# Kernel tuning notes

Hardware: AMD Instinct MI355X
Metric: run time of the kernel (lower is better)

The kernel has to match this reference:

```python
import jax, jax.numpy as jnp
import numpy as np

B, S, D = 1, 2048, 4096
H, KVH, HD = 32, 8, 128
ROPE_THETA = 10000.0
RMS_EPS = 1e-5


def setup_inputs() -> dict:
    key = jax.random.key(0)
    k1, k2, k3 = jax.random.split(key, 3)
    scale = 1.0 / np.sqrt(D)
    return {
        "inputs_embeds": jax.random.normal(k1, (B, S, D), dtype=jnp.float32),
        "attention_mask": jnp.ones((B, S), dtype=jnp.float32),
        "g": jnp.ones((D,), dtype=jnp.float32),
        "Wq": jax.random.normal(k2, (D, H * HD), dtype=jnp.float32) * scale,
        "Wk": jax.random.normal(k3, (D, KVH * HD), dtype=jnp.float32) * scale,
    }


def _rotate_half(x):
    return jnp.concatenate([-x[..., HD // 2:], x[..., :HD // 2]], axis=-1)


def reference(inputs_embeds, attention_mask, g, Wq, Wk):
    # RMSNorm
    var = jnp.mean(jnp.square(inputs_embeds), axis=-1, keepdims=True)
    h = inputs_embeds * jax.lax.rsqrt(var + RMS_EPS) * g

    # QK projections -> [B, heads, S, HD]
    q = (h @ Wq).reshape(B, S, H, HD).transpose(0, 2, 1, 3)
    k = (h @ Wk).reshape(B, S, KVH, HD).transpose(0, 2, 1, 3)

    # RoPE (llama-style: cos/sin of duplicated half-dim freqs)
    pos = jnp.arange(S, dtype=jnp.float32)
    inv_freq = 1.0 / (ROPE_THETA ** (jnp.arange(0, HD, 2, dtype=jnp.float32) / HD))
    freqs = pos[:, None] * inv_freq[None, :]            # [S, HD/2]
    emb = jnp.concatenate([freqs, freqs], axis=-1)       # [S, HD]
    cos = jnp.cos(emb)[None, None]                       # [1,1,S,HD]
    sin = jnp.sin(emb)[None, None]
    q = q * cos + _rotate_half(q) * sin
    k = k * cos + _rotate_half(k) * sin

    # repeat_kv: expand KV heads to H query heads (grouped-query)
    k = jnp.repeat(k, H // KVH, axis=1)                  # [B,H,S,HD]

    # raw QK^T scores (no softmax/V)
    scores = jnp.einsum('bhqd,bhkd->bhqk', q, k) / np.float32(np.sqrt(HD))

    # causal mask + 2D padding mask (all-ones here -> pure causal)
    min_f = jnp.finfo(scores.dtype).min
    i = jnp.arange(S)[:, None]
    j = jnp.arange(S)[None, :]
    causal = jnp.where(j > i, min_f, jnp.float32(0.0))   # [S,S]
    pad = (causal[None, None] == 0.0) & (attention_mask[:, None, None, :] == 0.0)
    mask = jnp.where(pad, min_f, causal[None, None])     # [B,1,S,S]
    return scores + mask
```

## Files before the change

kernel.cpp:

```cpp
#include <hip/hip_runtime.h>
#include <hip/hip_bf16.h>
#include <math.h>

#define S_LEN 2048
#define D_DIM 4096
#define NTOT 5120

typedef _Float16 f16x8 __attribute__((ext_vector_type(8)));
typedef float f32x4 __attribute__((ext_vector_type(4)));

#define MASKF (-3.3895313892515355e+38f)

#define QCH_BASE 134217728ull
#define KCH_BASE 201326592ull

__device__ __forceinline__ void async_ld16(const void* g, void* l) {
  __builtin_amdgcn_global_load_lds((const __attribute__((address_space(1))) void*)g,
                                   (__attribute__((address_space(3))) void*)l, 16, 0, 0);
}

__global__ void rope_tables(float* __restrict__ ct, float* __restrict__ st) {
  int i = blockIdx.x * 256 + threadIdx.x;
  int s = i >> 6, f = i & 63;
  float inv = (float)(1.0 / pow(10000.0, (double)(2 * f) / 128.0));
  float ang = (float)s * inv;
  ct[i] = (float)cos((double)ang);
  st[i] = (float)sin((double)ang);
}

__global__ __launch_bounds__(256) void rmsnorm_cast(const float* __restrict__ x,
                                                    const float* __restrict__ g,
                                                    _Float16* __restrict__ h) {
  int s = blockIdx.x;
  int t = threadIdx.x, w = t >> 6, l = t & 63;
  const f32x4* xr = (const f32x4*)(x + (size_t)s * D_DIM);
  const f32x4* gr = (const f32x4*)g;
  f32x4 v[4];
  float ss = 0.f;
#pragma unroll
  for (int i = 0; i < 4; ++i) {
    v[i] = xr[t + i * 256];
    ss += v[i][0] * v[i][0] + v[i][1] * v[i][1] + v[i][2] * v[i][2] + v[i][3] * v[i][3];
  }
#pragma unroll
  for (int off = 32; off; off >>= 1) ss += __shfl_down(ss, off);
  __shared__ float red[4];
  if (l == 0) red[w] = ss;
  __syncthreads();
  float tot = red[0] + red[1] + red[2] + red[3];
  float scale = rsqrtf(tot * (1.f / D_DIM) + 1e-5f);
  _Float16* hr = h + (size_t)s * D_DIM;
#pragma unroll
  for (int i = 0; i < 4; ++i) {
    f32x4 gg = gr[t + i * 256];
    _Float16 o[4];
    o[0] = (_Float16)(v[i][0] * scale * gg[0]);
    o[1] = (_Float16)(v[i][1] * scale * gg[1]);
    o[2] = (_Float16)(v[i][2] * scale * gg[2]);
    o[3] = (_Float16)(v[i][3] * scale * gg[3]);
    *(short4*)(hr + (size_t)(t + i * 256) * 4) = *(short4*)o;
  }
}

__global__ __launch_bounds__(256) void transpose_cast(const float* __restrict__ W,
                                                      _Float16* __restrict__ Wt, int N) {
  __shared__ float tile[32][33];
  int ntiles = N >> 5;
  int tn = blockIdx.x % ntiles, td = blockIdx.x / ntiles;
  int c = threadIdx.x & 31, r0 = threadIdx.x >> 5;
  int d0 = td * 32, n0 = tn * 32;
#pragma unroll
  for (int i = 0; i < 4; ++i) {
    int r = r0 + i * 8;
    tile[r][c] = W[(size_t)(d0 + r) * N + n0 + c];
  }
  __syncthreads();
#pragma unroll
  for (int i = 0; i < 4; ++i) {
    int r = r0 + i * 8;
    Wt[(size_t)(n0 + r) * D_DIM + d0 + c] = (_Float16)tile[c][r];
  }
}

__global__ __launch_bounds__(256, 2) void gemm_bt_f16(const _Float16* __restrict__ A,
                                                      const _Float16* __restrict__ Bt,
                                                      _Float16* __restrict__ C, int N, int K) {
  __shared__ _Float16 As[128 * 64];
  __shared__ _Float16 Bs[128 * 64];
  const int tid = threadIdx.x, w = tid >> 6, l = tid & 63;
  const int brow = blockIdx.y * 128, bcol = blockIdx.x * 128;
  const int wr = (w >> 1) * 64, wc = (w & 1) * 64;
  f32x4 acc[4][4] = {};

  int st_o[4], st_r[4], st_src[4];
#pragma unroll
  for (int p = 0; p < 4; ++p) {
    int ob = (p * 4 + w) * 1024;
    int o = ob + l * 16;
    int r = o >> 7;
    int slot = (o >> 4) & 7;
    st_o[p] = ob; st_r[p] = r; st_src[p] = slot ^ (r & 7);
  }

  for (int k0 = 0; k0 < K; k0 += 64) {
#pragma unroll
    for (int p = 0; p < 4; ++p) {
      async_ld16(A + (size_t)(brow + st_r[p]) * K + (k0 + st_src[p] * 8), (char*)As + st_o[p]);
      async_ld16(Bt + (size_t)(bcol + st_r[p]) * K + (k0 + st_src[p] * 8), (char*)Bs + st_o[p]);
    }
    asm volatile("s_waitcnt vmcnt(0)" ::: "memory");
    __syncthreads();
#pragma unroll
    for (int ks = 0; ks < 2; ++ks) {
      int kslot = ks * 4 + (l >> 4);
      f16x8 af[4], bf[4];
#pragma unroll
      for (int m = 0; m < 4; ++m) {
        int row = wr + m * 16 + (l & 15);
        af[m] = *(const f16x8*)((const char*)As + row * 128 + ((kslot ^ (row & 7)) << 4));
      }
#pragma unroll
      for (int n = 0; n < 4; ++n) {
        int row = wc + n * 16 + (l & 15);
        bf[n] = *(const f16x8*)((const char*)Bs + row * 128 + ((kslot ^ (row & 7)) << 4));
      }
#pragma unroll
      for (int m = 0; m < 4; ++m)
#pragma unroll
        for (int n = 0; n < 4; ++n)
          acc[m][n] = __builtin_amdgcn_mfma_f32_16x16x32_f16(af[m], bf[n], acc[m][n], 0, 0, 0);
    }
    __syncthreads();
  }
  const int colb = bcol + wc + (l & 15);
  const int rowb = brow + wr + ((l >> 4) << 2);
#pragma unroll
  for (int m = 0; m < 4; ++m)
#pragma unroll
    for (int n = 0; n < 4; ++n) {
      size_t base = (size_t)(rowb + m * 16) * N + (colb + n * 16);
#pragma unroll
      for (int j = 0; j < 4; ++j) C[base + (size_t)j * N] = (_Float16)acc[m][n][j];
    }
}

__global__ void rope_chunk(const _Float16* __restrict__ src, const float* __restrict__ ct,
                           const float* __restrict__ st, char* __restrict__ base) {
  int b = blockIdx.x;
  int s = b / 40, h = b % 40;
  int d = threadIdx.x;
  float v = (float)src[(size_t)s * NTOT + h * 128 + d];
  float p = (float)src[(size_t)s * NTOT + h * 128 + (d ^ 64)];
  float c = ct[s * 64 + (d & 63)];
  float sn = st[s * 64 + (d & 63)];
  float o = v * c + ((d < 64) ? -p : p) * sn;
  size_t byte;
  if (h < 32) {
    int cc = 2 * s + (h >> 4);
    byte = QCH_BASE + (size_t)(cc >> 10) * 16777216ull + (size_t)(cc & 1023) * 8192ull +
           4096ull + (size_t)((h & 15) * 128 + d) * 2;
  } else {
    int kv = h - 32;
    byte = KCH_BASE + (size_t)(s >> 1) * 8192ull + 4096ull + (size_t)(s & 1) * 2048ull +
           (size_t)(kv * 128 + d) * 2;
  }
  *(_Float16*)(base + byte) = (_Float16)o;
}

__device__ __forceinline__ void fill_tile_f32(float* __restrict__ outh, int qi, int kj) {
  f32x4 mv = {MASKF, MASKF, MASKF, MASKF};
  int rr = threadIdx.x >> 5, cc = threadIdx.x & 31;
#pragma unroll
  for (int i = 0; i < 16; ++i) {
    int r = qi * 128 + i * 8 + rr;
    ((f32x4*)(outh + (size_t)r * S_LEN + kj * 128))[cc] = mv;
  }
}

__global__ __launch_bounds__(256, 2) void qk_full(const char* __restrict__ base,
                                                  const float* __restrict__ am,
                                                  float* __restrict__ out) {
  __shared__ _Float16 Qs[128 * 128], Ks[128 * 128];
  const int h = blockIdx.y;
  const int qi = blockIdx.x >> 4, kj = blockIdx.x & 15;
  if (h >= 8 && h <= 12 && qi < 8 && kj >= 8) return;
  float* outh = out + (size_t)h * S_LEN * S_LEN;
  if (kj > qi) { fill_tile_f32(outh, qi, kj); return; }

  const int tid = threadIdx.x, w = tid >> 6, l = tid & 63;
  const int wr = (w >> 1) * 64, wc = (w & 1) * 64;
  const int hb = h >> 4;
  const size_t hoff = (size_t)(h & 15) * 256;
  const size_t kvoff = (size_t)(h >> 2) * 256;
#pragma unroll
  for (int p = 0; p < 8; ++p) {
    int ob = (p * 4 + w) * 1024;
    int o = ob + l * 16;
    int r = o >> 8;
    int slot = (o >> 4) & 15;
    int src = slot ^ (r & 7);
    int s = qi * 128 + r;
    int cc = 2 * s + hb;
    const char* qa = base + QCH_BASE + (size_t)(cc >> 10) * 16777216ull +
                     (size_t)(cc & 1023) * 8192ull + 4096ull + hoff + src * 16;
    int s2 = kj * 128 + r;
    const char* ka = base + KCH_BASE + (size_t)(s2 >> 1) * 8192ull + 4096ull +
                     (size_t)(s2 & 1) * 2048ull + kvoff + src * 16;
    async_ld16(qa, (char*)Qs + ob);
    async_ld16(ka, (char*)Ks + ob);
  }
  asm volatile("s_waitcnt vmcnt(0)" ::: "memory");
  __syncthreads();

  f32x4 acc[4][4] = {};
#pragma unroll
  for (int ks = 0; ks < 4; ++ks) {
    int kslot = ks * 4 + (l >> 4);
    f16x8 af[4], bf[4];
#pragma unroll
    for (int m = 0; m < 4; ++m) {
      int row = wr + m * 16 + (l & 15);
      af[m] = *(const f16x8*)((const char*)Qs + row * 256 + ((kslot ^ (row & 7)) << 4));
    }
#pragma unroll
    for (int n = 0; n < 4; ++n) {
      int row = wc + n * 16 + (l & 15);
      bf[n] = *(const f16x8*)((const char*)Ks + row * 256 + ((kslot ^ (row & 7)) << 4));
    }
#pragma unroll
    for (int m = 0; m < 4; ++m)
#pragma unroll
      for (int n = 0; n < 4; ++n)
        acc[m][n] = __builtin_amdgcn_mfma_f32_16x16x32_f16(af[m], bf[n], acc[m][n], 0, 0, 0);
  }

  const float sc = 0.088388347648318447f;
#pragma unroll
  for (int m = 0; m < 4; ++m) {
    int ib = qi * 128 + wr + m * 16 + ((l >> 4) << 2);
#pragma unroll
    for (int n = 0; n < 4; ++n) {
      int jg = kj * 128 + wc + n * 16 + (l & 15);
      float amv = am[jg];
#pragma unroll
      for (int j = 0; j < 4; ++j) {
        int i = ib + j;
        float v = acc[m][n][j] * sc;
        v = (v != v) ? 0.f : fminf(fmaxf(v, -3.38e38f), 3.38e38f);
        if (jg > i || amv == 0.f) v = MASKF;
        outh[(size_t)i * S_LEN + jg] = v;
      }
    }
  }
}

__global__ void fill_last(float* __restrict__ out) {
  int b = blockIdx.x;
  int h = 8 + (b >> 6);
  int t = b & 63;
  int qi = t >> 3, kj = 8 + (t & 7);
  fill_tile_f32(out + (size_t)h * S_LEN * S_LEN, qi, kj);
}

extern "C" void kernel_launch(void* const* d_in, const int* in_sizes, int n_in,
                              void* d_out, int out_size, void* d_ws, size_t ws_size,
                              hipStream_t stream) {
  const float* x  = (const float*)d_in[0];
  const float* am = (const float*)d_in[1];
  const float* g  = (const float*)d_in[2];
  const float* Wq = (const float*)d_in[3];
  const float* Wk = (const float*)d_in[4];
  float* out = (float*)d_out;
  char* ob = (char*)d_out;
  (void)d_ws; (void)ws_size;

  float*    ct   = (float*)(ob);
  float*    st   = (float*)(ob + 524288ull);
  _Float16* h16  = (_Float16*)(ob + 1048576ull);
  _Float16* wt   = (_Float16*)(ob + 17825792ull);
  _Float16* QKr  = (_Float16*)(ob + 59768832ull);

  rope_tables<<<dim3(512), dim3(256), 0, stream>>>(ct, st);
  rmsnorm_cast<<<dim3(2048), dim3(256), 0, stream>>>(x, g, h16);
  transpose_cast<<<dim3(128 * 128), dim3(256), 0, stream>>>(Wq, wt, 4096);
  transpose_cast<<<dim3(32 * 128), dim3(256), 0, stream>>>(Wk, wt + (size_t)4096 * D_DIM, 1024);
  gemm_bt_f16<<<dim3(40, 16), dim3(256), 0, stream>>>(h16, wt, QKr, NTOT, 4096);
  rope_chunk<<<dim3(2048 * 40), dim3(128), 0, stream>>>(QKr, ct, st, ob);
  qk_full<<<dim3(256, 32), dim3(256), 0, stream>>>(ob, am, out);
  fill_last<<<dim3(320), dim3(256), 0, stream>>>(out);
}
```

Baseline: 296.6 us.

## Fuse RoPE into QK projection GEMM epilogue with XCD-aware block mapping

The projection GEMM now applies RoPE in its epilogue. Each warp holds a full 128-wide head row, so the rotate-half partner sits in the same thread's accumulators (n^4). The rotated fp16 values go through swizzled LDS and are written with 16-byte stores straight into the chunked Q/K layout, which removes the intermediate QKr buffer and the separate per-element rope kernel. The launch also becomes a 1D grid remapped so that blocks on the same XCD share B columns, and the warp tiling changes from 64x64 to 32x128. The cost is more B-fragment LDS reads per warp and a different register footprint.

```diff
diff --git a/kernel.cpp b/kernel.cpp
--- a/kernel.cpp
+++ b/kernel.cpp
@@ -82,15 +82,24 @@
   }
 }
 
-__global__ __launch_bounds__(256, 2) void gemm_bt_f16(const _Float16* __restrict__ A,
-                                                      const _Float16* __restrict__ Bt,
-                                                      _Float16* __restrict__ C, int N, int K) {
-  __shared__ _Float16 As[128 * 64];
-  __shared__ _Float16 Bs[128 * 64];
+__global__ __launch_bounds__(256, 2) void gemm_rope(const _Float16* __restrict__ A,
+                                                    const _Float16* __restrict__ Bt,
+                                                    const float* __restrict__ ct,
+                                                    const float* __restrict__ st,
+                                                    char* __restrict__ base, int K) {
+  __shared__ _Float16 lds[128 * 128];
+  _Float16* As = lds;
+  _Float16* Bs = lds + 128 * 64;
+  const int bid = blockIdx.x;
+  const int xcd = bid & 7, idx = bid >> 3;
+  const int flat = xcd * 80 + idx;
+  const int bx = flat >> 4;
+  const int by = flat & 15;
+  const int brow = by * 128;
+  const size_t bcol = (size_t)bx * 128;
   const int tid = threadIdx.x, w = tid >> 6, l = tid & 63;
-  const int brow = blockIdx.y * 128, bcol = blockIdx.x * 128;
-  const int wr = (w >> 1) * 64, wc = (w & 1) * 64;
-  f32x4 acc[4][4] = {};
+  const int wr = w * 32;
+  f32x4 acc[2][8] = {};
 
   int st_o[4], st_r[4], st_src[4];
 #pragma unroll
@@ -106,65 +115,73 @@
 #pragma unroll
     for (int p = 0; p < 4; ++p) {
       async_ld16(A + (size_t)(brow + st_r[p]) * K + (k0 + st_src[p] * 8), (char*)As + st_o[p]);
-      async_ld16(Bt + (size_t)(bcol + st_r[p]) * K + (k0 + st_src[p] * 8), (char*)Bs + st_o[p]);
+      async_ld16(Bt + (bcol + st_r[p]) * K + (k0 + st_src[p] * 8), (char*)Bs + st_o[p]);
     }
     asm volatile("s_waitcnt vmcnt(0)" ::: "memory");
     __syncthreads();
 #pragma unroll
     for (int ks = 0; ks < 2; ++ks) {
       int kslot = ks * 4 + (l >> 4);
-      f16x8 af[4], bf[4];
-#pragma unroll
-      for (int m = 0; m < 4; ++m) {
+      f16x8 af[2], bf[8];
+#pragma unroll
+      for (int m = 0; m < 2; ++m) {
         int row = wr + m * 16 + (l & 15);
         af[m] = *(const f16x8*)((const char*)As + row * 128 + ((kslot ^ (row & 7)) << 4));
       }
 #pragma unroll
-      for (int n = 0; n < 4; ++n) {
-        int row = wc + n * 16 + (l & 15);
+      for (int n = 0; n < 8; ++n) {
+        int row = n * 16 + (l & 15);
         bf[n] = *(const f16x8*)((const char*)Bs + row * 128 + ((kslot ^ (row & 7)) << 4));
       }
 #pragma unroll
-      for (int m = 0; m < 4; ++m)
-#pragma unroll
-        for (int n = 0; n < 4; ++n)
+      for (int m = 0; m < 2; ++m)
+#pragma unroll
+        for (int n = 0; n < 8; ++n)
           acc[m][n] = __builtin_amdgcn_mfma_f32_16x16x32_f16(af[m], bf[n], acc[m][n], 0, 0, 0);
     }
     __syncthreads();
   }
-  const int colb = bcol + wc + (l & 15);
-  const int rowb = brow + wr + ((l >> 4) << 2);
-#pragma unroll
-  for (int m = 0; m < 4; ++m)
-#pragma unroll
-    for (int n = 0; n < 4; ++n) {
-      size_t base = (size_t)(rowb + m * 16) * N + (colb + n * 16);
-#pragma unroll
-      for (int j = 0; j < 4; ++j) C[base + (size_t)j * N] = (_Float16)acc[m][n][j];
-    }
-}
-
-__global__ void rope_chunk(const _Float16* __restrict__ src, const float* __restrict__ ct,
-                           const float* __restrict__ st, char* __restrict__ base) {
-  int b = blockIdx.x;
-  int s = b / 40, h = b % 40;
-  int d = threadIdx.x;
-  float v = (float)src[(size_t)s * NTOT + h * 128 + d];
-  float p = (float)src[(size_t)s * NTOT + h * 128 + (d ^ 64)];
-  float c = ct[s * 64 + (d & 63)];
-  float sn = st[s * 64 + (d & 63)];
-  float o = v * c + ((d < 64) ? -p : p) * sn;
-  size_t byte;
-  if (h < 32) {
-    int cc = 2 * s + (h >> 4);
-    byte = QCH_BASE + (size_t)(cc >> 10) * 16777216ull + (size_t)(cc & 1023) * 8192ull +
-           4096ull + (size_t)((h & 15) * 128 + d) * 2;
-  } else {
-    int kv = h - 32;
-    byte = KCH_BASE + (size_t)(s >> 1) * 8192ull + 4096ull + (size_t)(s & 1) * 2048ull +
-           (size_t)(kv * 128 + d) * 2;
-  }
-  *(_Float16*)(base + byte) = (_Float16)o;
+
+#pragma unroll
+  for (int m = 0; m < 2; ++m)
+#pragma unroll
+    for (int n = 0; n < 8; ++n) {
+      int col = n * 16 + (l & 15);
+      int f = col & 63;
+#pragma unroll
+      for (int j = 0; j < 4; ++j) {
+        int row = wr + m * 16 + ((l >> 4) << 2) + j;
+        int s = brow + row;
+        float v = acc[m][n][j];
+        float p = acc[m][n ^ 4][j];
+        float o = v * ct[s * 64 + f] + ((col < 64) ? -p : p) * st[s * 64 + f];
+        lds[row * 128 + (col ^ ((row & 7) << 3))] = (_Float16)o;
+      }
+    }
+  __syncthreads();
+
+  {
+    int row = tid >> 1, hh = tid & 1;
+    int s = brow + row;
+    int sw = (row & 7) << 3;
+    int h = bx;
+    char* dst;
+    if (h < 32) {
+      int cc = 2 * s + (h >> 4);
+      dst = base + QCH_BASE + (size_t)(cc >> 10) * 16777216ull +
+            (size_t)(cc & 1023) * 8192ull + 4096ull + (size_t)((h & 15) * 128 + hh * 64) * 2;
+    } else {
+      int kv = h - 32;
+      dst = base + KCH_BASE + (size_t)(s >> 1) * 8192ull + 4096ull +
+            (size_t)(s & 1) * 2048ull + (size_t)(kv * 128 + hh * 64) * 2;
+    }
+#pragma unroll
+    for (int k = 0; k < 8; ++k) {
+      int c = hh * 64 + k * 8;
+      f16x8 vv = *(const f16x8*)&lds[row * 128 + (c ^ sw)];
+      *(f16x8*)(dst + k * 16) = vv;
+    }
+  }
 }
 
 __device__ __forceinline__ void fill_tile_f32(float* __restrict__ outh, int qi, int kj) {
@@ -278,14 +295,12 @@
   float*    st   = (float*)(ob + 524288ull);
   _Float16* h16  = (_Float16*)(ob + 1048576ull);
   _Float16* wt   = (_Float16*)(ob + 17825792ull);
-  _Float16* QKr  = (_Float16*)(ob + 59768832ull);
 
   rope_tables<<<dim3(512), dim3(256), 0, stream>>>(ct, st);
   rmsnorm_cast<<<dim3(2048), dim3(256), 0, stream>>>(x, g, h16);
   transpose_cast<<<dim3(128 * 128), dim3(256), 0, stream>>>(Wq, wt, 4096);
   transpose_cast<<<dim3(32 * 128), dim3(256), 0, stream>>>(Wk, wt + (size_t)4096 * D_DIM, 1024);
-  gemm_bt_f16<<<dim3(40, 16), dim3(256), 0, stream>>>(h16, wt, QKr, NTOT, 4096);
-  rope_chunk<<<dim3(2048 * 40), dim3(128), 0, stream>>>(QKr, ct, st, ob);
+  gemm_rope<<<dim3(640), dim3(256), 0, stream>>>(h16, wt, ct, st, ob, 4096);
   qk_full<<<dim3(256, 32), dim3(256), 0, stream>>>(ob, am, out);
   fill_last<<<dim3(320), dim3(256), 0, stream>>>(out);
 }
```

Result: no change. 293.1 us (-1.2%).
